# Kernel tuning notes

Measured on AMD Instinct MI355X. Metric: run time of the kernel, lower is better.

The kernel has to match this reference:

```python
import jax, jax.numpy as jnp
import numpy as np

D_MODEL = 768
N_HEAD = 12
HEAD_DIM = D_MODEL // N_HEAD
SCALE = HEAD_DIM ** -0.5
B, T = 8, 1024
NEG_INF = -1e9


def setup_inputs() -> dict:
    key = jax.random.key(0)
    ks = jax.random.split(key, 4)
    x = jax.random.normal(ks[0], (B, T, D_MODEL), dtype=jnp.float32)
    W_attn = jax.random.normal(ks[1], (D_MODEL, 3 * D_MODEL), dtype=jnp.float32) * 0.02
    b_attn = jnp.zeros((3 * D_MODEL,), dtype=jnp.float32)
    W_proj = jax.random.normal(ks[2], (D_MODEL, D_MODEL), dtype=jnp.float32) * 0.02
    b_proj = jnp.zeros((D_MODEL,), dtype=jnp.float32)
    return {"x": x, "W_attn": W_attn, "b_attn": b_attn, "W_proj": W_proj, "b_proj": b_proj}


def reference(x, W_attn, b_attn, W_proj, b_proj):
    Bn, Tn, C = x.shape
    # fused QKV projection: [B,T,3C]
    qkv = jnp.einsum('btc,cd->btd', x, W_attn) + b_attn
    q, k, v = jnp.split(qkv, 3, axis=-1)
    # [B, H, T, hd]
    def heads(t):
        return t.reshape(Bn, Tn, N_HEAD, HEAD_DIM).transpose(0, 2, 1, 3)
    q, k, v = heads(q), heads(k), heads(v)
    # scaled dot-product scores [B,H,T,T]
    att = jnp.einsum('bhqd,bhkd->bhqk', q, k) * SCALE
    # causal mask: mask[i,j]=1 where j>i (upper triangle, excluded)
    causal = jnp.tril(jnp.ones((Tn, Tn), dtype=bool))
    att = jnp.where(causal[None, None, :, :], att, NEG_INF)
    att = jax.nn.softmax(att, axis=-1)
    # weighted value sum -> merge heads
    y = jnp.einsum('bhqk,bhkd->bhqd', att, v)
    y = y.transpose(0, 2, 1, 3).reshape(Bn, Tn, C)
    # output projection
    return jnp.einsum('btc,cd->btd', y, W_proj) + b_proj
```

## Files before the change

kernel.cpp:

```cpp
#include <hip/hip_runtime.h>
#include <hip/hip_bf16.h>

#define T_SEQ 1024
#define NBATCH 8
#define NHEAD 12
#define HD 64
#define CDIM 768
#define C3 2304
#define ATT_SCALE 0.125f

typedef __attribute__((ext_vector_type(8))) __bf16 bf16x8;
typedef __attribute__((ext_vector_type(4))) __bf16 bf16x4;
typedef __attribute__((ext_vector_type(2))) __bf16 bf16x2;
typedef __attribute__((ext_vector_type(4))) float  f32x4;
typedef __attribute__((ext_vector_type(16))) float f32x16;

__device__ __forceinline__ f32x4 mfma_bf16(bf16x8 a, bf16x8 b, f32x4 c) {
    return __builtin_amdgcn_mfma_f32_16x16x32_bf16(a, b, c, 0, 0, 0);
}
__device__ __forceinline__ f32x16 mfma32(bf16x8 a, bf16x8 b, f32x16 c) {
    return __builtin_amdgcn_mfma_f32_32x32x16_bf16(a, b, c, 0, 0, 0);
}

__device__ __forceinline__ void gload16(const void* g, void* l) {
    __builtin_amdgcn_global_load_lds(
        (const __attribute__((address_space(1))) unsigned int*)g,
        (__attribute__((address_space(3))) unsigned int*)l, 16, 0, 0);
}

#define WAIT_VM(N)  asm volatile("s_waitcnt vmcnt(" #N ")" ::: "memory")
#define WAIT_LGKM0  asm volatile("s_waitcnt lgkmcnt(0)" ::: "memory")

__global__ __launch_bounds__(256) void cvt_f32_bf16(const float* __restrict__ in,
                                                    __bf16* __restrict__ out, int n4) {
    int i = blockIdx.x * 256 + threadIdx.x;
    if (i < n4) {
        float4 v = ((const float4*)in)[i];
        bf16x4 o = { (__bf16)v.x, (__bf16)v.y, (__bf16)v.z, (__bf16)v.w };
        ((bf16x4*)out)[i] = o;
    }
}

__global__ __launch_bounds__(256) void transpose_cvt(const float* __restrict__ W,
                                                     __bf16* __restrict__ Wt,
                                                     int R, int C) {
    __shared__ float tile[32][33];
    const int c0 = blockIdx.x * 32, r0 = blockIdx.y * 32;
    const int tc = threadIdx.x & 31, tr = threadIdx.x >> 5;
#pragma unroll
    for (int i = 0; i < 4; ++i)
        tile[tr + i * 8][tc] = W[(size_t)(r0 + tr + i * 8) * C + c0 + tc];
    __syncthreads();
#pragma unroll
    for (int i = 0; i < 4; ++i)
        Wt[(size_t)(c0 + tr + i * 8) * R + r0 + tc] = (__bf16)tile[tc][tr + i * 8];
}

template<int OUT_BF16>
__global__ __launch_bounds__(256) void gemm_bt(const __bf16* __restrict__ A,
                                               const __bf16* __restrict__ Bt,
                                               const float* __restrict__ bias,
                                               void* __restrict__ Cout,
                                               int M, int N, int K, int nbx) {
    __shared__ __align__(16) __bf16 sA[3][128 * 32];
    __shared__ __align__(16) __bf16 sB[3][128 * 32];
    const int t = threadIdx.x, l = t & 63, w = t >> 6;
    const int l31 = l & 31, lh = l >> 5;
    const int wr = w >> 1, wc = w & 1;
    const int xcd = blockIdx.x & 7;
    const int local = blockIdx.x >> 3;
    const int m0 = (xcd * 8 + (local & 7)) * 128;
    const int n0 = (local >> 3) * 128;

    const int r_st = t >> 2;
    const int sw_st = (r_st & 3) ^ ((r_st >> 2) & 3);
    const int g_off = ((t & 3) ^ sw_st) << 3;
    const int sw_rd = (l31 & 3) ^ ((l31 >> 2) & 3);

    f32x16 acc[2][2];
#pragma unroll
    for (int m = 0; m < 2; ++m)
#pragma unroll
        for (int n = 0; n < 2; ++n)
#pragma unroll
            for (int r = 0; r < 16; ++r) acc[m][n][r] = 0.f;

    const int nk = K >> 5;

#pragma unroll
    for (int s = 0; s < 3; ++s) {
        const int k0 = s << 5;
#pragma unroll
        for (int i = 0; i < 2; ++i) {
            int r = i * 64 + r_st;
            gload16(A + (size_t)(m0 + r) * K + k0 + g_off,
                    (char*)&sA[s][0] + (i * 256 + w * 64) * 16);
            gload16(Bt + (size_t)(n0 + r) * K + k0 + g_off,
                    (char*)&sB[s][0] + (i * 256 + w * 64) * 16);
        }
    }

    int cur = 0;
    for (int kt = 0; kt < nk; ++kt) {
        if (kt + 2 < nk)      WAIT_VM(8);
        else if (kt + 1 < nk) WAIT_VM(4);
        else                  WAIT_VM(0);
        __builtin_amdgcn_s_barrier();

        bf16x8 af[2][2], bg[2][2];
#pragma unroll
        for (int m = 0; m < 2; ++m)
#pragma unroll
            for (int ks = 0; ks < 2; ++ks)
                af[m][ks] = *(const bf16x8*)(&sA[cur][(wr * 64 + m * 32 + l31) * 32
                                                      + ((((ks << 1) | lh) ^ sw_rd) << 3)]);
#pragma unroll
        for (int n = 0; n < 2; ++n)
#pragma unroll
            for (int ks = 0; ks < 2; ++ks)
                bg[n][ks] = *(const bf16x8*)(&sB[cur][(wc * 64 + n * 32 + l31) * 32
                                                      + ((((ks << 1) | lh) ^ sw_rd) << 3)]);

#pragma unroll
        for (int ks = 0; ks < 2; ++ks)
#pragma unroll
            for (int m = 0; m < 2; ++m)
#pragma unroll
                for (int n = 0; n < 2; ++n)
                    acc[m][n] = mfma32(af[m][ks], bg[n][ks], acc[m][n]);

        WAIT_LGKM0;
        __builtin_amdgcn_s_barrier();

        if (kt + 3 < nk) {
            const int k0 = (kt + 3) << 5;
#pragma unroll
            for (int i = 0; i < 2; ++i) {
                int r = i * 64 + r_st;
                gload16(A + (size_t)(m0 + r) * K + k0 + g_off,
                        (char*)&sA[cur][0] + (i * 256 + w * 64) * 16);
                gload16(Bt + (size_t)(n0 + r) * K + k0 + g_off,
                        (char*)&sB[cur][0] + (i * 256 + w * 64) * 16);
            }
        }
        cur = (cur == 2) ? 0 : cur + 1;
    }

#pragma unroll
    for (int n = 0; n < 2; ++n) {
        int col = n0 + wc * 64 + n * 32 + l31;
        float bv = bias[col];
#pragma unroll
        for (int m = 0; m < 2; ++m) {
            int rbase = m0 + wr * 64 + m * 32 + 4 * lh;
#pragma unroll
            for (int r = 0; r < 16; ++r) {
                int row = rbase + (r & 3) + 8 * (r >> 2);
                float v = acc[m][n][r] + bv;
                if (OUT_BF16)
                    ((__bf16*)Cout)[(size_t)row * N + col] = (__bf16)v;
                else
                    ((float*)Cout)[(size_t)row * N + col] = v;
            }
        }
    }
}

__global__ __launch_bounds__(256, 2) void attn_fwd(const __bf16* __restrict__ qkv,
                                                   __bf16* __restrict__ y) {
    const int tid = threadIdx.x, l = tid & 63, w = tid >> 6;
    const int lr = l & 15, lk = l >> 4;
    const int r7 = lr & 7;
    const int bid = blockIdx.x;
    const int pr = bid / 96;
    const int hb = bid % 96;
    const int h = hb % NHEAD;
    const int b = hb / NHEAD;

    __shared__ __align__(16) __bf16 sK[2][64][64];
    __shared__ __align__(16) __bf16 sV[2][64][64];
    __shared__ __align__(16) __bf16 sP[4][16][72];

    const size_t baseQ = (size_t)b * T_SEQ * C3 + h * HD;
    const __bf16* Kp = qkv + baseQ + CDIM;
    const __bf16* Vp = qkv + baseQ + 2 * CDIM;

    const int vk0 = tid >> 3;
    const int vc = (tid & 7) << 3;
    const int vg = tid & 7;
    const int krow = tid >> 3;
    const int kchunk = (tid & 7) ^ ((tid >> 3) & 7);

#pragma unroll 1
    for (int job = 0; job < 2; ++job) {
        const int qt = (job == 0) ? pr : 15 - pr;
        const int q0 = qt * 64;
        const int nt = qt + 1;
        const int q_abs = q0 + w * 16 + lr;

        const size_t rowQ = baseQ + (size_t)(q0 + w * 16 + lr) * C3;
        bf16x8 qa0 = *(const bf16x8*)(qkv + rowQ + lk * 8);
        bf16x8 qa1 = *(const bf16x8*)(qkv + rowQ + 32 + lk * 8);

        f32x4 acc[4];
#pragma unroll
        for (int fd = 0; fd < 4; ++fd) acc[fd] = f32x4{0.f, 0.f, 0.f, 0.f};
        float mrun = -1e30f, lrun = 0.f;

        bf16x8 vreg[2];
#pragma unroll
        for (int i = 0; i < 2; ++i)
            vreg[i] = *(const bf16x8*)(Vp + (size_t)(i * 32 + vk0) * C3 + vc);
#pragma unroll
        for (int i = 0; i < 2; ++i)
            gload16(Kp + (size_t)(i * 32 + krow) * C3 + kchunk * 8,
                    (char*)&sK[0][0][0] + (i * 256 + w * 64) * 16);
#pragma unroll
        for (int i = 0; i < 2; ++i) {
            int key = i * 32 + vk0;
#pragma unroll
            for (int e = 0; e < 8; ++e)
                sV[0][vc + e][key ^ ((e ^ vg) << 3)] = vreg[i][e];
        }
        __syncthreads();

#pragma unroll 1
        for (int t = 0; t < nt; ++t) {
            const int kv0 = t * 64;
            const int cur = t & 1, nxt = cur ^ 1;
            const bool pre = (t + 1 < nt);
            if (pre) {
                const int kvp = kv0 + 64;
#pragma unroll
                for (int i = 0; i < 2; ++i)
                    vreg[i] = *(const bf16x8*)(Vp + (size_t)(kvp + i * 32 + vk0) * C3 + vc);
#pragma unroll
                for (int i = 0; i < 2; ++i)
                    gload16(Kp + (size_t)(kvp + i * 32 + krow) * C3 + kchunk * 8,
                            (char*)&sK[nxt][0][0] + (i * 256 + w * 64) * 16);
            }
            f32x4 s[4];
            __builtin_amdgcn_s_setprio(1);
#pragma unroll
            for (int fc = 0; fc < 4; ++fc) {
                const __bf16* kr = &sK[cur][fc * 16 + lr][0];
                bf16x8 k0 = *(const bf16x8*)(kr + ((lk ^ r7) << 3));
                bf16x8 k1 = *(const bf16x8*)(kr + (((4 + lk) ^ r7) << 3));
                f32x4 z = f32x4{0.f, 0.f, 0.f, 0.f};
                z = mfma_bf16(k0, qa0, z);
                z = mfma_bf16(k1, qa1, z);
                s[fc] = z;
            }
            __builtin_amdgcn_s_setprio(0);
            float ps[4][4];
#pragma unroll
            for (int fc = 0; fc < 4; ++fc)
#pragma unroll
                for (int j = 0; j < 4; ++j) {
                    int key = kv0 + fc * 16 + lk * 4 + j;
                    ps[fc][j] = (key <= q_abs) ? s[fc][j] * ATT_SCALE : -1e30f;
                }
            float mt = -1e30f;
#pragma unroll
            for (int fc = 0; fc < 4; ++fc)
#pragma unroll
                for (int j = 0; j < 4; ++j) mt = fmaxf(mt, ps[fc][j]);
            mt = fmaxf(mt, __shfl_xor(mt, 16, 64));
            mt = fmaxf(mt, __shfl_xor(mt, 32, 64));
            const float mn = fmaxf(mrun, mt);
            const float corr = __expf(mrun - mn);
            mrun = mn;
            float rs = 0.f;
#pragma unroll
            for (int fc = 0; fc < 4; ++fc)
#pragma unroll
                for (int j = 0; j < 4; ++j) {
                    float p = __expf(ps[fc][j] - mn);
                    ps[fc][j] = p;
                    rs += p;
                }
            rs += __shfl_xor(rs, 16, 64);
            rs += __shfl_xor(rs, 32, 64);
            lrun = lrun * corr + rs;
            float cj[4];
#pragma unroll
            for (int j = 0; j < 4; ++j) cj[j] = __shfl(corr, lk * 4 + j, 64);
#pragma unroll
            for (int fd = 0; fd < 4; ++fd)
#pragma unroll
                for (int j = 0; j < 4; ++j) acc[fd][j] *= cj[j];
#pragma unroll
            for (int fc = 0; fc < 4; ++fc)
#pragma unroll
                for (int jp = 0; jp < 2; ++jp) {
                    bf16x2 pk = { (__bf16)ps[fc][jp * 2], (__bf16)ps[fc][jp * 2 + 1] };
                    *(bf16x2*)&sP[w][lr][fc * 16 + lk * 4 + jp * 2] = pk;
                }
            __builtin_amdgcn_s_setprio(1);
#pragma unroll
            for (int ks = 0; ks < 2; ++ks) {
                bf16x8 pa = *(const bf16x8*)&sP[w][lr][ks * 32 + lk * 8];
#pragma unroll
                for (int fd = 0; fd < 4; ++fd) {
                    int d = fd * 16 + lr;
                    int sw = ((d & 7) ^ ((d >> 3) & 7)) << 3;
                    bf16x8 vb = *(const bf16x8*)&sV[cur][d][(ks * 32 + lk * 8) ^ sw];
                    acc[fd] = mfma_bf16(pa, vb, acc[fd]);
                }
            }
            __builtin_amdgcn_s_setprio(0);
            if (pre) {
#pragma unroll
                for (int i = 0; i < 2; ++i) {
                    int key = i * 32 + vk0;
#pragma unroll
                    for (int e = 0; e < 8; ++e)
                        sV[nxt][vc + e][key ^ ((e ^ vg) << 3)] = vreg[i][e];
                }
            }
            __syncthreads();
        }

        float linv[4];
#pragma unroll
        for (int j = 0; j < 4; ++j) linv[j] = 1.f / __shfl(lrun, lk * 4 + j, 64);
        const size_t yrow0 = (size_t)(b * T_SEQ + q0 + w * 16 + lk * 4);
#pragma unroll
        for (int fd = 0; fd < 4; ++fd) {
            int col = h * HD + fd * 16 + lr;
#pragma unroll
            for (int j = 0; j < 4; ++j)
                y[(yrow0 + j) * CDIM + col] = (__bf16)(acc[fd][j] * linv[j]);
        }
    }
}

extern "C" void kernel_launch(void* const* d_in, const int* in_sizes, int n_in,
                              void* d_out, int out_size, void* d_ws, size_t ws_size,
                              hipStream_t stream) {
    const float* x      = (const float*)d_in[0];
    const float* W_attn = (const float*)d_in[1];
    const float* b_attn = (const float*)d_in[2];
    const float* W_proj = (const float*)d_in[3];
    const float* b_proj = (const float*)d_in[4];

    __bf16* xb  = (__bf16*)d_ws;
    __bf16* Wat = xb  + (size_t)8192 * 768;
    __bf16* Wpt = Wat + (size_t)2304 * 768;
    __bf16* qkv = Wpt + (size_t)768 * 768;
    __bf16* yb  = qkv + (size_t)8192 * 2304;

    cvt_f32_bf16<<<6144, 256, 0, stream>>>(x, xb, (8192 * 768) / 4);
    transpose_cvt<<<dim3(72, 24), 256, 0, stream>>>(W_attn, Wat, 768, 2304);
    transpose_cvt<<<dim3(24, 24), 256, 0, stream>>>(W_proj, Wpt, 768, 768);

    gemm_bt<1><<<18 * 64, 256, 0, stream>>>(xb, Wat, b_attn, (void*)qkv, 8192, 2304, 768, 18);
    attn_fwd<<<NBATCH * NHEAD * 8, 256, 0, stream>>>(qkv, yb);
    gemm_bt<0><<<6 * 64, 256, 0, stream>>>(yb, Wpt, b_proj, d_out, 8192, 768, 768, 6);
}
```

Measured before the change: 117.0 us.

## Replace QKV GEMM with B-panel-resident kernel streaming A from registers

Adds a dedicated QKV projection kernel in which each 512-thread block owns a 512x64 output tile. It stages half of the 64-column weight panel in LDS at a time, and each wave streams its A rows straight from global memory into registers, double-buffered across six K groups. This drops the A-side shared-memory staging and the per-K-step barriers of the generic tiled GEMM. In exchange it uses heavy register pressure, uncoalesced 16-byte A loads, scalar bf16 output stores, and fewer blocks (576) with only partial overlap of loads and MFMA.

```diff
diff --git a/kernel.cpp b/kernel.cpp
--- a/kernel.cpp
+++ b/kernel.cpp
@@ -54,6 +54,96 @@
 #pragma unroll
     for (int i = 0; i < 4; ++i)
         Wt[(size_t)(c0 + tr + i * 8) * R + r0 + tc] = (__bf16)tile[tc][tr + i * 8];
+}
+
+#define GRP(g, AC, AN)                                                         \
+    do {                                                                       \
+        if ((g) + 1 < 6) {                                                     \
+            _Pragma("unroll")                                                  \
+            for (int s = 0; s < 8; ++s) {                                      \
+                AN[0][s] = *(const bf16x8*)(pA0 + ((g) + 1) * 128 + s * 16);   \
+                AN[1][s] = *(const bf16x8*)(pA1 + ((g) + 1) * 128 + s * 16);   \
+            }                                                                  \
+        }                                                                      \
+        _Pragma("unroll")                                                      \
+        for (int s = 0; s < 8; ++s) {                                          \
+            int ls = ((g) % 3) * 8 + s;                                        \
+            bf16x8 b0 = *(const bf16x8*)&sB[((ls * 2 + lh) * 64 + l31) * 8];   \
+            bf16x8 b1 = *(const bf16x8*)&sB[((ls * 2 + lh) * 64 + 32 + l31) * 8]; \
+            acc[0][0] = mfma32(AC[0][s], b0, acc[0][0]);                       \
+            acc[0][1] = mfma32(AC[0][s], b1, acc[0][1]);                       \
+            acc[1][0] = mfma32(AC[1][s], b0, acc[1][0]);                       \
+            acc[1][1] = mfma32(AC[1][s], b1, acc[1][1]);                       \
+        }                                                                      \
+    } while (0)
+
+__global__ __launch_bounds__(512) void gemm_qkv_bp(const __bf16* __restrict__ A,
+                                                   const __bf16* __restrict__ Bt,
+                                                   const float* __restrict__ bias,
+                                                   __bf16* __restrict__ C) {
+    __shared__ __align__(16) __bf16 sB[48 * 64 * 8];
+    const int t = threadIdx.x, l = t & 63, w = t >> 6;
+    const int l31 = l & 31, lh = l >> 5;
+    const int np = blockIdx.x % 36, mb = blockIdx.x / 36;
+    const int m0 = mb * 512, n0 = np * 64;
+
+    const __bf16* pA0 = A + (size_t)(m0 + w * 64 + l31) * CDIM + lh * 8;
+    const __bf16* pA1 = pA0 + 32 * CDIM;
+
+    f32x16 acc[2][2];
+#pragma unroll
+    for (int mf = 0; mf < 2; ++mf)
+#pragma unroll
+        for (int nh = 0; nh < 2; ++nh)
+#pragma unroll
+            for (int r = 0; r < 16; ++r) acc[mf][nh][r] = 0.f;
+
+    bf16x8 Af0[2][8], Af1[2][8];
+
+    const int scol = t >> 3, sc0 = (t & 7) * 6;
+#pragma unroll
+    for (int i = 0; i < 6; ++i) {
+        int c = sc0 + i;
+        *(bf16x8*)&sB[(c * 64 + scol) * 8] =
+            *(const bf16x8*)(Bt + (size_t)(n0 + scol) * CDIM + c * 8);
+    }
+#pragma unroll
+    for (int s = 0; s < 8; ++s) {
+        Af0[0][s] = *(const bf16x8*)(pA0 + s * 16);
+        Af0[1][s] = *(const bf16x8*)(pA1 + s * 16);
+    }
+    __syncthreads();
+
+    GRP(0, Af0, Af1);
+    GRP(1, Af1, Af0);
+    GRP(2, Af0, Af1);
+
+    __syncthreads();
+#pragma unroll
+    for (int i = 0; i < 6; ++i) {
+        int c = sc0 + i;
+        *(bf16x8*)&sB[(c * 64 + scol) * 8] =
+            *(const bf16x8*)(Bt + (size_t)(n0 + scol) * CDIM + (48 + c) * 8);
+    }
+    __syncthreads();
+
+    GRP(3, Af1, Af0);
+    GRP(4, Af0, Af1);
+    GRP(5, Af1, Af0);
+
+#pragma unroll
+    for (int mf = 0; mf < 2; ++mf)
+#pragma unroll
+        for (int nh = 0; nh < 2; ++nh) {
+            int col = n0 + nh * 32 + l31;
+            float bv = bias[col];
+            int rbase = m0 + w * 64 + mf * 32 + 4 * lh;
+#pragma unroll
+            for (int r = 0; r < 16; ++r) {
+                int row = rbase + (r & 3) + 8 * (r >> 2);
+                C[(size_t)row * C3 + col] = (__bf16)(acc[mf][nh][r] + bv);
+            }
+        }
 }
 
 template<int OUT_BF16>
@@ -354,7 +444,7 @@
     transpose_cvt<<<dim3(72, 24), 256, 0, stream>>>(W_attn, Wat, 768, 2304);
     transpose_cvt<<<dim3(24, 24), 256, 0, stream>>>(W_proj, Wpt, 768, 768);
 
-    gemm_bt<1><<<18 * 64, 256, 0, stream>>>(xb, Wat, b_attn, (void*)qkv, 8192, 2304, 768, 18);
+    gemm_qkv_bp<<<16 * 36, 512, 0, stream>>>(xb, Wat, b_attn, qkv);
     attn_fwd<<<NBATCH * NHEAD * 8, 256, 0, stream>>>(qkv, yb);
     gemm_bt<0><<<6 * 64, 256, 0, stream>>>(yb, Wpt, b_proj, d_out, 8192, 768, 768, 6);
 }
```

Result: slower. 165.8 us (+41.8%).

## Fold scale into Q, mask only diagonal tile, lazily rescale softmax, merge transposes

Applied to the files above, without the earlier changes.

Several attention-loop cuts: the softmax scale is folded into Q once per query tile, the causal mask runs only on the diagonal key tile, and the running-max rescale of the accumulators is skipped unless some row's max rises by more than a threshold. The two weight transpose launches are merged into one grid to save a launch. Scaling Q in bf16 is exact for a power-of-two factor. The lazy rescale lets exponentials reach up to e^8 before normalisation, which slightly loosens numerical headroom, and adds a wave-wide vote per tile.

```diff
diff --git a/kernel.cpp b/kernel.cpp
--- a/kernel.cpp
+++ b/kernel.cpp
@@ -7,7 +7,6 @@
 #define HD 64
 #define CDIM 768
 #define C3 2304
-#define ATT_SCALE 0.125f
 
 typedef __attribute__((ext_vector_type(8))) __bf16 bf16x8;
 typedef __attribute__((ext_vector_type(4))) __bf16 bf16x4;
@@ -41,11 +40,16 @@
     }
 }
 
-__global__ __launch_bounds__(256) void transpose_cvt(const float* __restrict__ W,
-                                                     __bf16* __restrict__ Wt,
-                                                     int R, int C) {
+__global__ __launch_bounds__(256) void transpose_cvt2(const float* __restrict__ Wa,
+                                                      __bf16* __restrict__ Wat,
+                                                      const float* __restrict__ Wp,
+                                                      __bf16* __restrict__ Wpt) {
     __shared__ float tile[32][33];
-    const int c0 = blockIdx.x * 32, r0 = blockIdx.y * 32;
+    const int bx = blockIdx.x;
+    const float* W;  __bf16* Wt;  int C, c0;
+    if (bx < 72) { W = Wa; Wt = Wat; C = 2304; c0 = bx * 32; }
+    else         { W = Wp; Wt = Wpt; C = 768;  c0 = (bx - 72) * 32; }
+    const int r0 = blockIdx.y * 32;
     const int tc = threadIdx.x & 31, tr = threadIdx.x >> 5;
 #pragma unroll
     for (int i = 0; i < 4; ++i)
@@ -53,7 +57,7 @@
     __syncthreads();
 #pragma unroll
     for (int i = 0; i < 4; ++i)
-        Wt[(size_t)(c0 + tr + i * 8) * R + r0 + tc] = (__bf16)tile[tc][tr + i * 8];
+        Wt[(size_t)(c0 + tr + i * 8) * 768 + r0 + tc] = (__bf16)tile[tc][tr + i * 8];
 }
 
 template<int OUT_BF16>
@@ -201,6 +205,11 @@
         const size_t rowQ = baseQ + (size_t)(q0 + w * 16 + lr) * C3;
         bf16x8 qa0 = *(const bf16x8*)(qkv + rowQ + lk * 8);
         bf16x8 qa1 = *(const bf16x8*)(qkv + rowQ + 32 + lk * 8);
+#pragma unroll
+        for (int e = 0; e < 8; ++e) {
+            qa0[e] = (__bf16)((float)qa0[e] * 0.125f);
+            qa1[e] = (__bf16)((float)qa1[e] * 0.125f);
+        }
 
         f32x4 acc[4];
 #pragma unroll
@@ -256,39 +265,48 @@
 #pragma unroll
             for (int fc = 0; fc < 4; ++fc)
 #pragma unroll
-                for (int j = 0; j < 4; ++j) {
-                    int key = kv0 + fc * 16 + lk * 4 + j;
-                    ps[fc][j] = (key <= q_abs) ? s[fc][j] * ATT_SCALE : -1e30f;
-                }
-            float mt = -1e30f;
+                for (int j = 0; j < 4; ++j) ps[fc][j] = s[fc][j];
+            if (t == nt - 1) {
+#pragma unroll
+                for (int fc = 0; fc < 4; ++fc)
+#pragma unroll
+                    for (int j = 0; j < 4; ++j) {
+                        int key = kv0 + fc * 16 + lk * 4 + j;
+                        if (key > q_abs) ps[fc][j] = -1e30f;
+                    }
+            }
+            float mfc[4];
 #pragma unroll
             for (int fc = 0; fc < 4; ++fc)
-#pragma unroll
-                for (int j = 0; j < 4; ++j) mt = fmaxf(mt, ps[fc][j]);
+                mfc[fc] = fmaxf(fmaxf(ps[fc][0], ps[fc][1]), fmaxf(ps[fc][2], ps[fc][3]));
+            float mt = fmaxf(fmaxf(mfc[0], mfc[1]), fmaxf(mfc[2], mfc[3]));
             mt = fmaxf(mt, __shfl_xor(mt, 16, 64));
             mt = fmaxf(mt, __shfl_xor(mt, 32, 64));
-            const float mn = fmaxf(mrun, mt);
-            const float corr = __expf(mrun - mn);
-            mrun = mn;
+            if (!__all(mt - mrun <= 8.f)) {
+                const float mn = fmaxf(mrun, mt);
+                const float corr = __expf(mrun - mn);
+                mrun = mn;
+                lrun *= corr;
+                float cj[4];
+#pragma unroll
+                for (int j = 0; j < 4; ++j) cj[j] = __shfl(corr, lk * 4 + j, 64);
+#pragma unroll
+                for (int fd = 0; fd < 4; ++fd)
+#pragma unroll
+                    for (int j = 0; j < 4; ++j) acc[fd][j] *= cj[j];
+            }
             float rs = 0.f;
 #pragma unroll
             for (int fc = 0; fc < 4; ++fc)
 #pragma unroll
                 for (int j = 0; j < 4; ++j) {
-                    float p = __expf(ps[fc][j] - mn);
+                    float p = __expf(ps[fc][j] - mrun);
                     ps[fc][j] = p;
                     rs += p;
                 }
             rs += __shfl_xor(rs, 16, 64);
             rs += __shfl_xor(rs, 32, 64);
-            lrun = lrun * corr + rs;
-            float cj[4];
-#pragma unroll
-            for (int j = 0; j < 4; ++j) cj[j] = __shfl(corr, lk * 4 + j, 64);
-#pragma unroll
-            for (int fd = 0; fd < 4; ++fd)
-#pragma unroll
-                for (int j = 0; j < 4; ++j) acc[fd][j] *= cj[j];
+            lrun += rs;
 #pragma unroll
             for (int fc = 0; fc < 4; ++fc)
 #pragma unroll
@@ -351,8 +369,7 @@
     __bf16* yb  = qkv + (size_t)8192 * 2304;
 
     cvt_f32_bf16<<<6144, 256, 0, stream>>>(x, xb, (8192 * 768) / 4);
-    transpose_cvt<<<dim3(72, 24), 256, 0, stream>>>(W_attn, Wat, 768, 2304);
-    transpose_cvt<<<dim3(24, 24), 256, 0, stream>>>(W_proj, Wpt, 768, 768);
+    transpose_cvt2<<<dim3(96, 24), 256, 0, stream>>>(W_attn, Wat, W_proj, Wpt);
 
     gemm_bt<1><<<18 * 64, 256, 0, stream>>>(xb, Wat, b_attn, (void*)qkv, 8192, 2304, 768, 18);
     attn_fwd<<<NBATCH * NHEAD * 8, 256, 0, stream>>>(qkv, yb);
```

Result: faster. 111.7 us (-4.5%).
